# Kernel tuning notes

Measured on AMD Instinct MI355X. Metric: run time of the kernel, lower is better.

The kernel has to match this reference:

```python
import jax, jax.numpy as jnp
import numpy as np

LN_EPS = 1e-5

def _next_fast_len(n):
    # smallest 5-smooth integer >= n (matches scipy.fftpack.next_fast_len)
    while True:
        m = n
        for p in (2, 3, 5):
            while m % p == 0:
                m //= p
        if m == 1:
            return n
        n += 1

def _conv1d_fft(x, w):
    # x: (b, h, N, d), convolved along axis -2 against w: (h, M) along axis -1.
    # Matches the torch reference: multiply by conj(rfft(w)), roll by -1, take last N.
    N = x.shape[-2]
    M = w.shape[-1]
    L = _next_fast_len(N + M - 1)
    fx = jnp.fft.rfft(x, n=L, axis=-2)                    # (b, h, F, d) complex
    fw = jnp.fft.rfft(w, n=L, axis=-1)                    # (h, F) complex
    out = jnp.fft.irfft(fx * jnp.conj(fw)[..., None], L, axis=-2)
    out = jnp.roll(out, -1, axis=-2)
    return out[..., L - N:, :]                            # (b, h, N, d)

def setup_inputs() -> dict:
    key = jax.random.key(0)
    ks = jax.random.split(key, 5)
    b, n, d, h = 4, 4096, 1024, 8
    dh = d // h
    s = 0.02
    return {
        "x": jax.random.normal(ks[0], (b, n, d), jnp.float32),
        "ln_gamma": jnp.ones((d,), jnp.float32),
        "ln_beta": jnp.zeros((d,), jnp.float32),
        "w_in": jax.random.normal(ks[1], (d, d), jnp.float32) * s,
        "b_in": jnp.zeros((d,), jnp.float32),
        "initial_state": jax.random.normal(ks[2], (h, dh), jnp.float32),
        "alpha": jax.random.normal(ks[3], (h,), jnp.float32),
        "w_out": jax.random.normal(ks[4], (d, d), jnp.float32) * s,
        "b_out": jnp.zeros((d,), jnp.float32),
    }

def reference(x, ln_gamma, ln_beta, w_in, b_in, initial_state, alpha, w_out, b_out):
    b, n, d = x.shape
    h, dh = initial_state.shape
    # LayerNorm
    mu = jnp.mean(x, axis=-1, keepdims=True)
    var = jnp.mean((x - mu) ** 2, axis=-1, keepdims=True)
    xn = (x - mu) * jax.lax.rsqrt(var + LN_EPS) * ln_gamma + ln_beta
    # project_in (torch Linear: y = x @ W.T + b)
    xp = xn @ w_in.T + b_in
    # b n (h d) -> b h n d
    xh = xp.reshape(b, n, h, dh).transpose(0, 2, 1, 3)
    # prepend learned initial state, then first difference along n
    init = jnp.broadcast_to(initial_state[None, :, None, :], (b, h, 1, dh))
    xc = jnp.concatenate([init, xh], axis=2)
    xd = xc[:, :, 1:] - xc[:, :, :-1]                     # (b, h, n, dh)
    # EMA weights per head
    a = jax.nn.sigmoid(alpha)[:, None]                    # (h, 1)
    ar = jnp.arange(n)
    w = a * (1.0 - a) ** ar[::-1]                         # (h, n)
    out = _conv1d_fft(xd, w)
    # initial-state contribution
    init_w = (1.0 - a) ** (ar + 1)                        # (h, n)
    out = out + init_w[:, :, None] * initial_state[:, None, :]
    # b h n d -> b n (h d), then project_out
    out = out.transpose(0, 2, 1, 3).reshape(b, n, d)
    return out @ w_out.T + b_out
```

## Files before the change

### kernel.cpp

```cpp
#include <hip/hip_runtime.h>
#include <stdint.h>

typedef float  f32x4 __attribute__((ext_vector_type(4)));
typedef __bf16 bf16x8 __attribute__((ext_vector_type(8)));
typedef short  s16x8 __attribute__((ext_vector_type(8)));
typedef unsigned short u16;

static __device__ __forceinline__ u16 f2bf(float f) {
  unsigned u = __float_as_uint(f);
  u += 0x7fffu + ((u >> 16) & 1u);
  return (u16)(u >> 16);
}
static __device__ __forceinline__ float bf2f(u16 u) {
  return __uint_as_float(((unsigned)u) << 16);
}

static __device__ __forceinline__ void async_copy16(void* lds, const void* g) {
  __builtin_amdgcn_global_load_lds(
      (const __attribute__((address_space(1))) unsigned int*)g,
      (__attribute__((address_space(3))) unsigned int*)lds, 16, 0, 0);
}

__global__ __launch_bounds__(256) void cvt_k(const float* __restrict__ in,
                                             u16* __restrict__ out, int n4) {
  int i = blockIdx.x * 256 + threadIdx.x;
  if (i >= n4) return;
  float4 v = reinterpret_cast<const float4*>(in)[i];
  ushort4 o;
  o.x = f2bf(v.x); o.y = f2bf(v.y); o.z = f2bf(v.z); o.w = f2bf(v.w);
  reinterpret_cast<ushort4*>(out)[i] = o;
}

__global__ __launch_bounds__(256) void ln_k(const float* __restrict__ x,
                                            const float* __restrict__ g,
                                            const float* __restrict__ b,
                                            u16* __restrict__ xn) {
  const int D = 1024;
  const int row = blockIdx.x;
  const int tid = threadIdx.x;
  const float4 v = reinterpret_cast<const float4*>(x + (size_t)row * D)[tid];
  float s  = v.x + v.y + v.z + v.w;
  float s2 = v.x * v.x + v.y * v.y + v.z * v.z + v.w * v.w;
  #pragma unroll
  for (int off = 32; off > 0; off >>= 1) {
    s  += __shfl_down(s, off);
    s2 += __shfl_down(s2, off);
  }
  __shared__ float red[8];
  const int lane = tid & 63, wv = tid >> 6;
  if (lane == 0) { red[wv] = s; red[4 + wv] = s2; }
  __syncthreads();
  s  = red[0] + red[1] + red[2] + red[3];
  s2 = red[4] + red[5] + red[6] + red[7];
  const float mu   = s * (1.0f / D);
  const float var  = s2 * (1.0f / D) - mu * mu;
  const float rstd = rsqrtf(var + 1e-5f);
  const float4 gv = reinterpret_cast<const float4*>(g)[tid];
  const float4 bv = reinterpret_cast<const float4*>(b)[tid];
  ushort4 o;
  o.x = f2bf((v.x - mu) * rstd * gv.x + bv.x);
  o.y = f2bf((v.y - mu) * rstd * gv.y + bv.y);
  o.z = f2bf((v.z - mu) * rstd * gv.z + bv.z);
  o.w = f2bf((v.w - mu) * rstd * gv.w + bv.w);
  reinterpret_cast<ushort4*>(xn + (size_t)row * D)[tid] = o;
}

template<int OUT_BF16>
__global__ __launch_bounds__(256) void gemm2_k(const u16* __restrict__ A,
                                               const u16* __restrict__ Bm,
                                               const float* __restrict__ bias,
                                               void* __restrict__ Cv,
                                               int M, int N, int K) {
  const int tid  = threadIdx.x;
  const int lane = tid & 63;
  const int wv   = tid >> 6;
  const int ntN  = N >> 7;
  const int nwg  = (M >> 7) * ntN;
  const int bid  = blockIdx.x;
  const int wgid = (bid & 7) * (nwg >> 3) + (bid >> 3);
  const int mt = wgid / ntN, nt = wgid % ntN;
  const int m0 = mt << 7, n0 = nt << 7;

  __shared__ __align__(16) u16 sA[2][128 * 64];
  __shared__ __align__(16) u16 sB[2][128 * 64];

  const int trow = tid >> 3;
  const int tch  = tid & 7;
  const int csw  = (tch ^ (trow & 7)) << 3;
  const u16* gA = A  + (size_t)(m0 + trow) * K + csw;
  const u16* gB = Bm + (size_t)(n0 + trow) * K + csw;
  const int lofs = trow * 64 + (tch << 3);

  f32x4 acc[4][4];
  #pragma unroll
  for (int i = 0; i < 4; ++i)
    #pragma unroll
    for (int j = 0; j < 4; ++j) acc[i][j] = f32x4{0.f, 0.f, 0.f, 0.f};

  const int wr  = (wv >> 1) << 6;
  const int wc  = (wv & 1) << 6;
  const int fr  = lane & 15;
  const int fkc = lane >> 4;
  const int sx  = fr & 7;

  const int nk = K >> 6;
  int buf = 0;

  #pragma unroll
  for (int r = 0; r < 4; ++r) {
    async_copy16(&sA[0][lofs + r * 2048], gA + (size_t)r * 32 * K);
    async_copy16(&sB[0][lofs + r * 2048], gB + (size_t)r * 32 * K);
  }
  __syncthreads();

  for (int t = 0; t < nk; ++t) {
    if (t + 1 < nk) {
      const size_t ko = (size_t)(t + 1) << 6;
      #pragma unroll
      for (int r = 0; r < 4; ++r) {
        async_copy16(&sA[buf ^ 1][lofs + r * 2048], gA + ko + (size_t)r * 32 * K);
        async_copy16(&sB[buf ^ 1][lofs + r * 2048], gB + ko + (size_t)r * 32 * K);
      }
    }
    const u16* bA = sA[buf];
    const u16* bB = sB[buf];
    #pragma unroll
    for (int s = 0; s < 2; ++s) {
      const int ch = ((((s << 2) + fkc) ^ sx) << 3);
      s16x8 af[4], bfr[4];
      #pragma unroll
      for (int i = 0; i < 4; ++i)
        af[i] = *reinterpret_cast<const s16x8*>(&bA[(wr + i * 16 + fr) * 64 + ch]);
      #pragma unroll
      for (int j = 0; j < 4; ++j)
        bfr[j] = *reinterpret_cast<const s16x8*>(&bB[(wc + j * 16 + fr) * 64 + ch]);
      #pragma unroll
      for (int i = 0; i < 4; ++i)
        #pragma unroll
        for (int j = 0; j < 4; ++j)
          acc[i][j] = __builtin_amdgcn_mfma_f32_16x16x32_bf16(
              __builtin_bit_cast(bf16x8, af[i]),
              __builtin_bit_cast(bf16x8, bfr[j]), acc[i][j], 0, 0, 0);
    }
    __syncthreads();
    buf ^= 1;
  }

  const int cr = (lane >> 4) << 2;
  const int cc = lane & 15;
  #pragma unroll
  for (int j = 0; j < 4; ++j) {
    const int col = n0 + wc + j * 16 + cc;
    const float bv = bias[col];
    #pragma unroll
    for (int i = 0; i < 4; ++i) {
      #pragma unroll
      for (int rr = 0; rr < 4; ++rr) {
        const int row = m0 + wr + i * 16 + cr + rr;
        const float val = acc[i][j][rr] + bv;
        if (OUT_BF16) ((u16*)Cv)[(size_t)row * N + col] = f2bf(val);
        else          ((float*)Cv)[(size_t)row * N + col] = val;
      }
    }
  }
}

__global__ __launch_bounds__(256) void ema_chunk_k(const u16* __restrict__ xp,
                                                   const float* __restrict__ alpha,
                                                   const float* __restrict__ init,
                                                   float* __restrict__ carry) {
  const int Nn = 4096, Dd = 1024, T = 128, nCh = 32;
  int bid = blockIdx.x;
  const int cg = bid & 1;  bid >>= 1;
  const int q  = bid & 31; bid >>= 5;
  const int bb = bid;
  const int c = cg * 512 + threadIdx.x * 2;
  const int h = c >> 7;
  const float a = 1.0f / (1.0f + __expf(-alpha[h]));
  const float r = 1.0f - a;
  const u16* px = xp + ((size_t)bb * Nn + (size_t)q * T) * Dd + c;
  float p0, p1;
  if (q == 0) { p0 = init[c]; p1 = init[c + 1]; }
  else { ushort2 pv = *(const ushort2*)(px - Dd); p0 = bf2f(pv.x); p1 = bf2f(pv.y); }
  float L0 = 0.f, L1 = 0.f;
  #pragma unroll 4
  for (int t = 0; t < T; ++t) {
    ushort2 v = *(const ushort2*)(px + (size_t)t * Dd);
    float v0 = bf2f(v.x), v1 = bf2f(v.y);
    L0 = r * L0 + a * (v0 - p0);
    L1 = r * L1 + a * (v1 - p1);
    p0 = v0; p1 = v1;
  }
  *(float2*)(carry + ((size_t)bb * nCh + q) * Dd + c) = make_float2(L0, L1);
}

__global__ __launch_bounds__(256) void ema_carry_k(const float* __restrict__ alpha,
                                                   const float* __restrict__ init,
                                                   float* __restrict__ carry) {
  const int Dd = 1024, nCh = 32;
  const int idx = blockIdx.x * 256 + threadIdx.x;
  const int c  = idx & (Dd - 1);
  const int bb = idx >> 10;
  const int h = c >> 7;
  const float a = 1.0f / (1.0f + __expf(-alpha[h]));
  const float r = 1.0f - a;
  float rT = r;
  #pragma unroll
  for (int s = 0; s < 7; ++s) rT *= rT;
  float L[32];
  #pragma unroll
  for (int q = 0; q < nCh; ++q)
    L[q] = carry[((size_t)bb * nCh + q) * Dd + c];
  float cin = init[c];
  #pragma unroll
  for (int q = 0; q < nCh; ++q) {
    carry[((size_t)bb * nCh + q) * Dd + c] = cin;
    cin = rT * cin + L[q];
  }
}

__global__ __launch_bounds__(256) void ema_apply_k(const u16* __restrict__ xp,
                                                   const float* __restrict__ alpha,
                                                   const float* __restrict__ init,
                                                   const float* __restrict__ carry,
                                                   u16* __restrict__ ob) {
  const int Nn = 4096, Dd = 1024, T = 128, nCh = 32;
  int bid = blockIdx.x;
  const int cg = bid & 1;  bid >>= 1;
  const int q  = bid & 31; bid >>= 5;
  const int bb = bid;
  const int c = cg * 512 + threadIdx.x * 2;
  const int h = c >> 7;
  const float a = 1.0f / (1.0f + __expf(-alpha[h]));
  const float r = 1.0f - a;
  const u16* px = xp + ((size_t)bb * Nn + (size_t)q * T) * Dd + c;
  u16* po = ob + ((size_t)bb * Nn + (size_t)q * T) * Dd + c;
  float2 Oin = *(const float2*)(carry + ((size_t)bb * nCh + q) * Dd + c);
  float O0 = Oin.x, O1 = Oin.y;
  float p0, p1;
  if (q == 0) { p0 = init[c]; p1 = init[c + 1]; }
  else { ushort2 pv = *(const ushort2*)(px - Dd); p0 = bf2f(pv.x); p1 = bf2f(pv.y); }
  #pragma unroll 4
  for (int t = 0; t < T; ++t) {
    ushort2 v = *(const ushort2*)(px + (size_t)t * Dd);
    float v0 = bf2f(v.x), v1 = bf2f(v.y);
    O0 = r * O0 + a * (v0 - p0);
    O1 = r * O1 + a * (v1 - p1);
    p0 = v0; p1 = v1;
    ushort2 o; o.x = f2bf(O0); o.y = f2bf(O1);
    *(ushort2*)(po + (size_t)t * Dd) = o;
  }
}

extern "C" void kernel_launch(void* const* d_in, const int* in_sizes, int n_in,
                              void* d_out, int out_size, void* d_ws, size_t ws_size,
                              hipStream_t stream) {
  const float* x     = (const float*)d_in[0];
  const float* ln_g  = (const float*)d_in[1];
  const float* ln_b  = (const float*)d_in[2];
  const float* w_in  = (const float*)d_in[3];
  const float* b_in  = (const float*)d_in[4];
  const float* init  = (const float*)d_in[5];
  const float* alpha = (const float*)d_in[6];
  const float* w_out = (const float*)d_in[7];
  const float* b_out = (const float*)d_in[8];
  float* out = (float*)d_out;

  const int B = 4, N = 4096, D = 1024;
  const int M = B * N;

  char* p = (char*)d_ws;
  u16*   xn  = (u16*)p; p += (size_t)M * D * sizeof(u16);
  u16*   wi  = (u16*)p; p += (size_t)D * D * sizeof(u16);
  u16*   wo  = (u16*)p; p += (size_t)D * D * sizeof(u16);
  u16*   xpb = (u16*)p; p += (size_t)M * D * sizeof(u16);
  float* cr  = (float*)p; p += (size_t)B * 32 * D * sizeof(float);
  u16*   ob  = (u16*)p;

  const int n4 = D * D / 4;
  cvt_k<<<dim3((n4 + 255) / 256), dim3(256), 0, stream>>>(w_in, wi, n4);
  cvt_k<<<dim3((n4 + 255) / 256), dim3(256), 0, stream>>>(w_out, wo, n4);
  ln_k<<<dim3(M), dim3(256), 0, stream>>>(x, ln_g, ln_b, xn);
  gemm2_k<1><<<dim3((M / 128) * (D / 128)), dim3(256), 0, stream>>>(xn, wi, b_in, xpb, M, D, D);
  ema_chunk_k<<<dim3(B * 32 * 2), dim3(256), 0, stream>>>(xpb, alpha, init, cr);
  ema_carry_k<<<dim3(B * D / 256), dim3(256), 0, stream>>>(alpha, init, cr);
  ema_apply_k<<<dim3(B * 32 * 2), dim3(256), 0, stream>>>(xpb, alpha, init, cr, ob);
  gemm2_k<0><<<dim3((M / 128) * (D / 128)), dim3(256), 0, stream>>>(ob, wo, b_out, out, M, D, D);
}
```

Before: 155.0 us.

## Replace 128x128 GEMM with 256x256 eight-wave tile and interleaved prefetch

Both projection GEMMs move from a 128x128 tile with 4 waves to a 256x256 tile with 8 waves, each wave owning a 128x64 sub-tile. The K loop is split into four phases that interleave LDS fragment loads, async global-to-LDS prefetch of the next K slice, and MFMA blocks. Raw barriers and s_setprio bracket each MFMA block. The aim is more data reuse per LDS byte and more overlap of loads with matrix math. The cost is more LDS per block, higher register pressure from 32 accumulators, and only 256 workgroups per GEMM, which may underfill the CUs.

```diff
diff --git a/kernel.cpp b/kernel.cpp
--- a/kernel.cpp
+++ b/kernel.cpp
@@ -65,24 +65,32 @@
   reinterpret_cast<ushort4*>(xn + (size_t)row * D)[tid] = o;
 }
 
+static __device__ __forceinline__ s16x8 ldfrag(const u16* b, int row, int ks,
+                                               int fkc, int sx) {
+  return *reinterpret_cast<const s16x8*>(
+      &b[row * 64 + ((((ks << 2) + fkc) ^ sx) << 3)]);
+}
+
 template<int OUT_BF16>
-__global__ __launch_bounds__(256) void gemm2_k(const u16* __restrict__ A,
-                                               const u16* __restrict__ Bm,
-                                               const float* __restrict__ bias,
-                                               void* __restrict__ Cv,
-                                               int M, int N, int K) {
+__global__ __launch_bounds__(512, 2) void gemm8_k(const u16* __restrict__ A,
+                                                  const u16* __restrict__ Bm,
+                                                  const float* __restrict__ bias,
+                                                  void* __restrict__ Cv,
+                                                  int M, int N, int K) {
   const int tid  = threadIdx.x;
   const int lane = tid & 63;
   const int wv   = tid >> 6;
-  const int ntN  = N >> 7;
-  const int nwg  = (M >> 7) * ntN;
+  const int wrr  = wv >> 2;
+  const int wcc  = wv & 3;
+  const int ntN  = N >> 8;
+  const int nwg  = (M >> 8) * ntN;
   const int bid  = blockIdx.x;
   const int wgid = (bid & 7) * (nwg >> 3) + (bid >> 3);
   const int mt = wgid / ntN, nt = wgid % ntN;
-  const int m0 = mt << 7, n0 = nt << 7;
-
-  __shared__ __align__(16) u16 sA[2][128 * 64];
-  __shared__ __align__(16) u16 sB[2][128 * 64];
+  const int m0 = mt << 8, n0 = nt << 8;
+
+  __shared__ __align__(16) u16 sA[2][256 * 64];
+  __shared__ __align__(16) u16 sB[2][256 * 64];
 
   const int trow = tid >> 3;
   const int tch  = tid & 7;
@@ -91,73 +99,150 @@
   const u16* gB = Bm + (size_t)(n0 + trow) * K + csw;
   const int lofs = trow * 64 + (tch << 3);
 
-  f32x4 acc[4][4];
-  #pragma unroll
-  for (int i = 0; i < 4; ++i)
+  f32x4 acc[8][4];
+  #pragma unroll
+  for (int i = 0; i < 8; ++i)
     #pragma unroll
     for (int j = 0; j < 4; ++j) acc[i][j] = f32x4{0.f, 0.f, 0.f, 0.f};
 
-  const int wr  = (wv >> 1) << 6;
-  const int wc  = (wv & 1) << 6;
   const int fr  = lane & 15;
   const int fkc = lane >> 4;
   const int sx  = fr & 7;
-
-  const int nk = K >> 6;
-  int buf = 0;
+  const int abase = wrr << 7;
+  const int bbase = wcc << 6;
+
+  const int NK = K >> 6;
 
   #pragma unroll
   for (int r = 0; r < 4; ++r) {
-    async_copy16(&sA[0][lofs + r * 2048], gA + (size_t)r * 32 * K);
-    async_copy16(&sB[0][lofs + r * 2048], gB + (size_t)r * 32 * K);
-  }
-  __syncthreads();
-
-  for (int t = 0; t < nk; ++t) {
-    if (t + 1 < nk) {
-      const size_t ko = (size_t)(t + 1) << 6;
-      #pragma unroll
-      for (int r = 0; r < 4; ++r) {
-        async_copy16(&sA[buf ^ 1][lofs + r * 2048], gA + ko + (size_t)r * 32 * K);
-        async_copy16(&sB[buf ^ 1][lofs + r * 2048], gB + ko + (size_t)r * 32 * K);
-      }
-    }
-    const u16* bA = sA[buf];
-    const u16* bB = sB[buf];
-    #pragma unroll
-    for (int s = 0; s < 2; ++s) {
-      const int ch = ((((s << 2) + fkc) ^ sx) << 3);
-      s16x8 af[4], bfr[4];
-      #pragma unroll
-      for (int i = 0; i < 4; ++i)
-        af[i] = *reinterpret_cast<const s16x8*>(&bA[(wr + i * 16 + fr) * 64 + ch]);
-      #pragma unroll
-      for (int j = 0; j < 4; ++j)
-        bfr[j] = *reinterpret_cast<const s16x8*>(&bB[(wc + j * 16 + fr) * 64 + ch]);
-      #pragma unroll
-      for (int i = 0; i < 4; ++i)
+    async_copy16(&sA[0][lofs + r * 4096], gA + (size_t)r * 64 * K);
+    async_copy16(&sB[0][lofs + r * 4096], gB + (size_t)r * 64 * K);
+  }
+  asm volatile("s_waitcnt vmcnt(0)" ::: "memory");
+  __builtin_amdgcn_s_barrier();
+
+  s16x8 af[4][2], bfr[2][2];
+
+  for (int kt = 0; kt < NK; ++kt) {
+    const int cur = kt & 1;
+    const u16* bA = sA[cur];
+    const u16* bB = sB[cur];
+    u16* nA = sA[cur ^ 1];
+    u16* nB = sB[cur ^ 1];
+    const bool pf = (kt + 1 < NK);
+    const size_t ko = (size_t)(kt + 1) << 6;
+
+    #pragma unroll
+    for (int i = 0; i < 4; ++i)
+      #pragma unroll
+      for (int ks = 0; ks < 2; ++ks)
+        af[i][ks] = ldfrag(bA, abase + i * 16 + fr, ks, fkc, sx);
+    #pragma unroll
+    for (int j = 0; j < 2; ++j)
+      #pragma unroll
+      for (int ks = 0; ks < 2; ++ks)
+        bfr[j][ks] = ldfrag(bB, bbase + j * 16 + fr, ks, fkc, sx);
+    if (pf) {
+      async_copy16(&nA[lofs], gA + ko);
+      async_copy16(&nA[lofs + 4096], gA + ko + (size_t)64 * K);
+    }
+    __builtin_amdgcn_s_barrier();
+    __builtin_amdgcn_s_setprio(1);
+    #pragma unroll
+    for (int i = 0; i < 4; ++i)
+      #pragma unroll
+      for (int j = 0; j < 2; ++j)
         #pragma unroll
-        for (int j = 0; j < 4; ++j)
+        for (int ks = 0; ks < 2; ++ks)
           acc[i][j] = __builtin_amdgcn_mfma_f32_16x16x32_bf16(
-              __builtin_bit_cast(bf16x8, af[i]),
-              __builtin_bit_cast(bf16x8, bfr[j]), acc[i][j], 0, 0, 0);
-    }
-    __syncthreads();
-    buf ^= 1;
+              __builtin_bit_cast(bf16x8, af[i][ks]),
+              __builtin_bit_cast(bf16x8, bfr[j][ks]), acc[i][j], 0, 0, 0);
+    __builtin_amdgcn_s_setprio(0);
+    __builtin_amdgcn_s_barrier();
+
+    #pragma unroll
+    for (int j = 0; j < 2; ++j)
+      #pragma unroll
+      for (int ks = 0; ks < 2; ++ks)
+        bfr[j][ks] = ldfrag(bB, bbase + 32 + j * 16 + fr, ks, fkc, sx);
+    if (pf) {
+      async_copy16(&nA[lofs + 2 * 4096], gA + ko + (size_t)128 * K);
+      async_copy16(&nA[lofs + 3 * 4096], gA + ko + (size_t)192 * K);
+    }
+    __builtin_amdgcn_s_barrier();
+    __builtin_amdgcn_s_setprio(1);
+    #pragma unroll
+    for (int i = 0; i < 4; ++i)
+      #pragma unroll
+      for (int j = 0; j < 2; ++j)
+        #pragma unroll
+        for (int ks = 0; ks < 2; ++ks)
+          acc[i][2 + j] = __builtin_amdgcn_mfma_f32_16x16x32_bf16(
+              __builtin_bit_cast(bf16x8, af[i][ks]),
+              __builtin_bit_cast(bf16x8, bfr[j][ks]), acc[i][2 + j], 0, 0, 0);
+    __builtin_amdgcn_s_setprio(0);
+    __builtin_amdgcn_s_barrier();
+
+    #pragma unroll
+    for (int i = 0; i < 4; ++i)
+      #pragma unroll
+      for (int ks = 0; ks < 2; ++ks)
+        af[i][ks] = ldfrag(bA, abase + 64 + i * 16 + fr, ks, fkc, sx);
+    if (pf) {
+      async_copy16(&nB[lofs], gB + ko);
+      async_copy16(&nB[lofs + 4096], gB + ko + (size_t)64 * K);
+    }
+    __builtin_amdgcn_s_barrier();
+    __builtin_amdgcn_s_setprio(1);
+    #pragma unroll
+    for (int i = 0; i < 4; ++i)
+      #pragma unroll
+      for (int j = 0; j < 2; ++j)
+        #pragma unroll
+        for (int ks = 0; ks < 2; ++ks)
+          acc[4 + i][2 + j] = __builtin_amdgcn_mfma_f32_16x16x32_bf16(
+              __builtin_bit_cast(bf16x8, af[i][ks]),
+              __builtin_bit_cast(bf16x8, bfr[j][ks]), acc[4 + i][2 + j], 0, 0, 0);
+    __builtin_amdgcn_s_setprio(0);
+    __builtin_amdgcn_s_barrier();
+
+    #pragma unroll
+    for (int j = 0; j < 2; ++j)
+      #pragma unroll
+      for (int ks = 0; ks < 2; ++ks)
+        bfr[j][ks] = ldfrag(bB, bbase + j * 16 + fr, ks, fkc, sx);
+    if (pf) {
+      async_copy16(&nB[lofs + 2 * 4096], gB + ko + (size_t)128 * K);
+      async_copy16(&nB[lofs + 3 * 4096], gB + ko + (size_t)192 * K);
+    }
+    __builtin_amdgcn_s_barrier();
+    __builtin_amdgcn_s_setprio(1);
+    #pragma unroll
+    for (int i = 0; i < 4; ++i)
+      #pragma unroll
+      for (int j = 0; j < 2; ++j)
+        #pragma unroll
+        for (int ks = 0; ks < 2; ++ks)
+          acc[4 + i][j] = __builtin_amdgcn_mfma_f32_16x16x32_bf16(
+              __builtin_bit_cast(bf16x8, af[i][ks]),
+              __builtin_bit_cast(bf16x8, bfr[j][ks]), acc[4 + i][j], 0, 0, 0);
+    __builtin_amdgcn_s_setprio(0);
+    if (pf) asm volatile("s_waitcnt vmcnt(0)" ::: "memory");
+    __builtin_amdgcn_s_barrier();
   }
 
   const int cr = (lane >> 4) << 2;
   const int cc = lane & 15;
   #pragma unroll
-  for (int j = 0; j < 4; ++j) {
-    const int col = n0 + wc + j * 16 + cc;
+  for (int nj = 0; nj < 4; ++nj) {
+    const int col = n0 + (wcc << 6) + nj * 16 + cc;
     const float bv = bias[col];
     #pragma unroll
-    for (int i = 0; i < 4; ++i) {
+    for (int mi = 0; mi < 8; ++mi) {
       #pragma unroll
       for (int rr = 0; rr < 4; ++rr) {
-        const int row = m0 + wr + i * 16 + cr + rr;
-        const float val = acc[i][j][rr] + bv;
+        const int row = m0 + (wrr << 7) + mi * 16 + cr + rr;
+        const float val = acc[mi][nj][rr] + bv;
         if (OUT_BF16) ((u16*)Cv)[(size_t)row * N + col] = f2bf(val);
         else          ((float*)Cv)[(size_t)row * N + col] = val;
       }
@@ -281,9 +366,9 @@
   cvt_k<<<dim3((n4 + 255) / 256), dim3(256), 0, stream>>>(w_in, wi, n4);
   cvt_k<<<dim3((n4 + 255) / 256), dim3(256), 0, stream>>>(w_out, wo, n4);
   ln_k<<<dim3(M), dim3(256), 0, stream>>>(x, ln_g, ln_b, xn);
-  gemm2_k<1><<<dim3((M / 128) * (D / 128)), dim3(256), 0, stream>>>(xn, wi, b_in, xpb, M, D, D);
+  gemm8_k<1><<<dim3((M / 256) * (D / 256)), dim3(512), 0, stream>>>(xn, wi, b_in, xpb, M, D, D);
   ema_chunk_k<<<dim3(B * 32 * 2), dim3(256), 0, stream>>>(xpb, alpha, init, cr);
   ema_carry_k<<<dim3(B * D / 256), dim3(256), 0, stream>>>(alpha, init, cr);
   ema_apply_k<<<dim3(B * 32 * 2), dim3(256), 0, stream>>>(xpb, alpha, init, cr, ob);
-  gemm2_k<0><<<dim3((M / 128) * (D / 128)), dim3(256), 0, stream>>>(ob, wo, b_out, out, M, D, D);
-}
+  gemm8_k<0><<<dim3((M / 256) * (D / 256)), dim3(512), 0, stream>>>(ob, wo, b_out, out, M, D, D);
+}
```

New measurement: 153.8 us. About the same (-0.8%).

## Fuse EMA chunk reduction into input GEMM epilogue and stage stores via LDS

Applied to the files above, without the earlier changes.

The input-projection GEMM now stages its output tile in shared memory, writes it with coalesced vector stores, and computes the per-chunk EMA partial sums directly from the fp32 tile. This removes the separate ema_chunk pass that re-read the projected activations. The carry kernel fixes up the first-difference term at chunk boundaries using bf16 values, and the two weight conversion launches are merged into one. The cost is extra LDS traffic and a sync in the GEMM epilogue, plus a small numerical change because the partial sums now use fp32 values instead of bf16-rounded ones.

```diff
diff --git a/kernel.cpp b/kernel.cpp
--- a/kernel.cpp
+++ b/kernel.cpp
@@ -21,14 +21,18 @@
       (__attribute__((address_space(3))) unsigned int*)lds, 16, 0, 0);
 }
 
-__global__ __launch_bounds__(256) void cvt_k(const float* __restrict__ in,
-                                             u16* __restrict__ out, int n4) {
+__global__ __launch_bounds__(256) void cvt2_k(const float* __restrict__ in0,
+                                              const float* __restrict__ in1,
+                                              u16* __restrict__ out0,
+                                              u16* __restrict__ out1, int n4) {
   int i = blockIdx.x * 256 + threadIdx.x;
-  if (i >= n4) return;
-  float4 v = reinterpret_cast<const float4*>(in)[i];
+  const float* in = (i < n4) ? in0 : in1;
+  u16* out = (i < n4) ? out0 : out1;
+  int idx = (i < n4) ? i : i - n4;
+  float4 v = reinterpret_cast<const float4*>(in)[idx];
   ushort4 o;
   o.x = f2bf(v.x); o.y = f2bf(v.y); o.z = f2bf(v.z); o.w = f2bf(v.w);
-  reinterpret_cast<ushort4*>(out)[i] = o;
+  reinterpret_cast<ushort4*>(out)[idx] = o;
 }
 
 __global__ __launch_bounds__(256) void ln_k(const float* __restrict__ x,
@@ -65,12 +69,14 @@
   reinterpret_cast<ushort4*>(xn + (size_t)row * D)[tid] = o;
 }
 
-template<int OUT_BF16>
-__global__ __launch_bounds__(256) void gemm2_k(const u16* __restrict__ A,
-                                               const u16* __restrict__ Bm,
-                                               const float* __restrict__ bias,
-                                               void* __restrict__ Cv,
-                                               int M, int N, int K) {
+template<int MODE>
+__global__ __launch_bounds__(256) void gemm_bt_k(const u16* __restrict__ A,
+                                                 const u16* __restrict__ Bm,
+                                                 const float* __restrict__ bias,
+                                                 void* __restrict__ Cv,
+                                                 const float* __restrict__ alpha,
+                                                 float* __restrict__ Lp,
+                                                 int M, int N, int K) {
   const int tid  = threadIdx.x;
   const int lane = tid & 63;
   const int wv   = tid >> 6;
@@ -81,8 +87,8 @@
   const int mt = wgid / ntN, nt = wgid % ntN;
   const int m0 = mt << 7, n0 = nt << 7;
 
-  __shared__ __align__(16) u16 sA[2][128 * 64];
-  __shared__ __align__(16) u16 sB[2][128 * 64];
+  __shared__ __align__(16) u16 smem[32768];
+  __shared__ float sRed[128];
 
   const int trow = tid >> 3;
   const int tch  = tid & 7;
@@ -108,22 +114,23 @@
 
   #pragma unroll
   for (int r = 0; r < 4; ++r) {
-    async_copy16(&sA[0][lofs + r * 2048], gA + (size_t)r * 32 * K);
-    async_copy16(&sB[0][lofs + r * 2048], gB + (size_t)r * 32 * K);
+    async_copy16(&smem[lofs + r * 2048], gA + (size_t)r * 32 * K);
+    async_copy16(&smem[16384 + lofs + r * 2048], gB + (size_t)r * 32 * K);
   }
   __syncthreads();
 
   for (int t = 0; t < nk; ++t) {
     if (t + 1 < nk) {
       const size_t ko = (size_t)(t + 1) << 6;
+      const int nb = (buf ^ 1) * 8192;
       #pragma unroll
       for (int r = 0; r < 4; ++r) {
-        async_copy16(&sA[buf ^ 1][lofs + r * 2048], gA + ko + (size_t)r * 32 * K);
-        async_copy16(&sB[buf ^ 1][lofs + r * 2048], gB + ko + (size_t)r * 32 * K);
+        async_copy16(&smem[nb + lofs + r * 2048], gA + ko + (size_t)r * 32 * K);
+        async_copy16(&smem[16384 + nb + lofs + r * 2048], gB + ko + (size_t)r * 32 * K);
       }
     }
-    const u16* bA = sA[buf];
-    const u16* bB = sB[buf];
+    const u16* bA = smem + buf * 8192;
+    const u16* bB = smem + 16384 + buf * 8192;
     #pragma unroll
     for (int s = 0; s < 2; ++s) {
       const int ch = ((((s << 2) + fkc) ^ sx) << 3);
@@ -146,55 +153,69 @@
     buf ^= 1;
   }
 
+  float* sC = (float*)smem;
   const int cr = (lane >> 4) << 2;
   const int cc = lane & 15;
-  #pragma unroll
-  for (int j = 0; j < 4; ++j) {
-    const int col = n0 + wc + j * 16 + cc;
-    const float bv = bias[col];
+  float bv[4];
+  #pragma unroll
+  for (int nj = 0; nj < 4; ++nj) bv[nj] = bias[n0 + wc + nj * 16 + cc];
+  #pragma unroll
+  for (int mi = 0; mi < 4; ++mi)
     #pragma unroll
-    for (int i = 0; i < 4; ++i) {
+    for (int nj = 0; nj < 4; ++nj)
       #pragma unroll
       for (int rr = 0; rr < 4; ++rr) {
-        const int row = m0 + wr + i * 16 + cr + rr;
-        const float val = acc[i][j][rr] + bv;
-        if (OUT_BF16) ((u16*)Cv)[(size_t)row * N + col] = f2bf(val);
-        else          ((float*)Cv)[(size_t)row * N + col] = val;
+        const int row = wr + mi * 16 + cr + rr;
+        const int col = wc + nj * 16 + cc;
+        sC[row * 128 + (col ^ ((row & 4) << 2))] = acc[mi][nj][rr] + bv[nj];
       }
-    }
-  }
-}
-
-__global__ __launch_bounds__(256) void ema_chunk_k(const u16* __restrict__ xp,
+  __syncthreads();
+  #pragma unroll 4
+  for (int it = 0; it < 16; ++it) {
+    const int row  = it * 8 + (tid >> 5);
+    const int col0 = (tid & 31) * 4;
+    f32x4 v = *(const f32x4*)&sC[row * 128 + (col0 ^ ((row & 4) << 2))];
+    const size_t goff = (size_t)(m0 + row) * N + n0 + col0;
+    if (MODE == 1) {
+      ushort4 o; o.x = f2bf(v[0]); o.y = f2bf(v[1]); o.z = f2bf(v[2]); o.w = f2bf(v[3]);
+      *(ushort4*)&((u16*)Cv)[goff] = o;
+    } else {
+      *(f32x4*)&((float*)Cv)[goff] = v;
+    }
+  }
+  if (MODE == 1) {
+    const int col = tid & 127;
+    const int hh = (n0 + col) >> 7;
+    const float a  = 1.0f / (1.0f + __expf(-alpha[hh]));
+    const float rw = 1.0f - a;
+    float r64 = rw;
+    #pragma unroll
+    for (int s = 0; s < 6; ++s) r64 *= r64;
+    const bool lo = (tid < 128);
+    const int rbase  = lo ? 1 : 64;
+    const int nsteps = lo ? 63 : 64;
+    float prev = sC[(rbase - 1) * 128 + (col ^ (((rbase - 1) & 4) << 2))];
+    float L = 0.f;
+    #pragma unroll 8
+    for (int t = rbase; t < rbase + 64; ++t) {
+      if (t - rbase >= nsteps) break;
+      const float w = sC[t * 128 + (col ^ ((t & 4) << 2))];
+      L = rw * L + a * (w - prev);
+      prev = w;
+    }
+    if (!lo) sRed[col] = L;
+    __syncthreads();
+    if (lo) {
+      const float Lt = r64 * L + sRed[col];
+      const int bb = m0 >> 12;
+      const int q  = (m0 >> 7) & 31;
+      Lp[((size_t)bb * 32 + q) * 1024 + n0 + col] = Lt;
+    }
+  }
+}
+
+__global__ __launch_bounds__(256) void ema_carry_k(const u16* __restrict__ xpb,
                                                    const float* __restrict__ alpha,
-                                                   const float* __restrict__ init,
-                                                   float* __restrict__ carry) {
-  const int Nn = 4096, Dd = 1024, T = 128, nCh = 32;
-  int bid = blockIdx.x;
-  const int cg = bid & 1;  bid >>= 1;
-  const int q  = bid & 31; bid >>= 5;
-  const int bb = bid;
-  const int c = cg * 512 + threadIdx.x * 2;
-  const int h = c >> 7;
-  const float a = 1.0f / (1.0f + __expf(-alpha[h]));
-  const float r = 1.0f - a;
-  const u16* px = xp + ((size_t)bb * Nn + (size_t)q * T) * Dd + c;
-  float p0, p1;
-  if (q == 0) { p0 = init[c]; p1 = init[c + 1]; }
-  else { ushort2 pv = *(const ushort2*)(px - Dd); p0 = bf2f(pv.x); p1 = bf2f(pv.y); }
-  float L0 = 0.f, L1 = 0.f;
-  #pragma unroll 4
-  for (int t = 0; t < T; ++t) {
-    ushort2 v = *(const ushort2*)(px + (size_t)t * Dd);
-    float v0 = bf2f(v.x), v1 = bf2f(v.y);
-    L0 = r * L0 + a * (v0 - p0);
-    L1 = r * L1 + a * (v1 - p1);
-    p0 = v0; p1 = v1;
-  }
-  *(float2*)(carry + ((size_t)bb * nCh + q) * Dd + c) = make_float2(L0, L1);
-}
-
-__global__ __launch_bounds__(256) void ema_carry_k(const float* __restrict__ alpha,
                                                    const float* __restrict__ init,
                                                    float* __restrict__ carry) {
   const int Dd = 1024, nCh = 32;
@@ -204,18 +225,20 @@
   const int h = c >> 7;
   const float a = 1.0f / (1.0f + __expf(-alpha[h]));
   const float r = 1.0f - a;
-  float rT = r;
-  #pragma unroll
-  for (int s = 0; s < 7; ++s) rT *= rT;
-  float L[32];
-  #pragma unroll
-  for (int q = 0; q < nCh; ++q)
-    L[q] = carry[((size_t)bb * nCh + q) * Dd + c];
+  float q_ = r, r127 = 1.0f;
+  #pragma unroll
+  for (int s = 0; s < 7; ++s) { r127 *= q_; q_ *= q_; }
+  const float rT = r127 * r;
   float cin = init[c];
-  #pragma unroll
+  float prevv = cin;
   for (int q = 0; q < nCh; ++q) {
-    carry[((size_t)bb * nCh + q) * Dd + c] = cin;
-    cin = rT * cin + L[q];
+    const size_t rowb = (size_t)bb * 4096 + (size_t)q * 128;
+    const float v0 = bf2f(xpb[rowb * Dd + c]);
+    const size_t off = ((size_t)bb * nCh + q) * Dd + c;
+    const float L = carry[off] + a * r127 * (v0 - prevv);
+    carry[off] = cin;
+    cin = rT * cin + L;
+    prevv = bf2f(xpb[(rowb + 127) * Dd + c]);
   }
 }
 
@@ -278,12 +301,12 @@
   u16*   ob  = (u16*)p;
 
   const int n4 = D * D / 4;
-  cvt_k<<<dim3((n4 + 255) / 256), dim3(256), 0, stream>>>(w_in, wi, n4);
-  cvt_k<<<dim3((n4 + 255) / 256), dim3(256), 0, stream>>>(w_out, wo, n4);
+  cvt2_k<<<dim3(2 * n4 / 256), dim3(256), 0, stream>>>(w_in, w_out, wi, wo, n4);
   ln_k<<<dim3(M), dim3(256), 0, stream>>>(x, ln_g, ln_b, xn);
-  gemm2_k<1><<<dim3((M / 128) * (D / 128)), dim3(256), 0, stream>>>(xn, wi, b_in, xpb, M, D, D);
-  ema_chunk_k<<<dim3(B * 32 * 2), dim3(256), 0, stream>>>(xpb, alpha, init, cr);
-  ema_carry_k<<<dim3(B * D / 256), dim3(256), 0, stream>>>(alpha, init, cr);
+  gemm_bt_k<1><<<dim3((M / 128) * (D / 128)), dim3(256), 0, stream>>>(
+      xn, wi, b_in, xpb, alpha, cr, M, D, D);
+  ema_carry_k<<<dim3(B * D / 256), dim3(256), 0, stream>>>(xpb, alpha, init, cr);
   ema_apply_k<<<dim3(B * 32 * 2), dim3(256), 0, stream>>>(xpb, alpha, init, cr, ob);
-  gemm2_k<0><<<dim3((M / 128) * (D / 128)), dim3(256), 0, stream>>>(ob, wo, b_out, out, M, D, D);
-}
+  gemm_bt_k<0><<<dim3((M / 128) * (D / 128)), dim3(256), 0, stream>>>(
+      ob, wo, b_out, out, nullptr, nullptr, M, D, D);
+}
```

After: 143.8 us. 1.08x faster.
